# Optimization experiments

Measured on AMD Instinct MI355X. Metric: run time of the kernel, lower is better.

Reference implementation:

```python
import jax, jax.numpy as jnp
import numpy as np

EPS = 1e-8

def setup_inputs() -> dict:
    key = jax.random.key(0)
    ks = jax.random.split(key, 8)
    B, D, N, F = 8192, 1024, 2048, 8
    d2 = D // 2
    # integer-valued data (IDF acts on integers)
    x = jnp.round(jax.random.normal(ks[0], (B, D), jnp.float32) * 5.0)
    s1 = 1.0 / np.sqrt(d2)
    s2 = 1.0 / np.sqrt(N)
    return {
        "x": x,
        "W1": jax.random.normal(ks[1], (F, d2, N), jnp.float32) * s1,
        "b1": jax.random.normal(ks[2], (F, N), jnp.float32) * 0.01,
        "W2": jax.random.normal(ks[3], (F, N, N), jnp.float32) * s2,
        "b2": jax.random.normal(ks[4], (F, N), jnp.float32) * 0.01,
        "W3": jax.random.normal(ks[5], (F, N, d2), jnp.float32) * s2,
        "b3": jax.random.normal(ks[6], (F, d2), jnp.float32) * 0.01,
        "mean": jnp.zeros((1, D), jnp.float32),
        "log_scale": jnp.ones((1, D), jnp.float32),
    }

def _st_round(v):
    # straight-through round: forward round, identity gradient
    return v + jax.lax.stop_gradient(jnp.round(v) - v)

def _flow(x, W1, b1, W2, b2, W3, b3):
    d2 = x.shape[1] // 2
    def step(z, p):
        w1, bb1, w2, bb2, w3, bb3 = p
        xa, xb = z[:, :d2], z[:, d2:]
        h = jax.nn.leaky_relu(xa @ w1 + bb1)          # [B, N]
        h = jax.nn.leaky_relu(h @ w2 + bb2)           # [B, N]
        t = h @ w3 + bb3                               # [B, d2]
        yb = xb + _st_round(t)
        z = jnp.concatenate([xa, yb], axis=1)[:, ::-1]  # coupling + flip permute
        return z, None
    z, _ = jax.lax.scan(step, x, (W1, b1, W2, b2, W3, b3))
    return z

def reference(x, W1, b1, W2, b2, W3, b3, mean, log_scale):
    z = _flow(x, W1, b1, W2, b2, W3, b3)
    # discretized logistic log-prior: log(sig((z+.5-m)/s) - sig((z-.5-m)/s))
    scale = jnp.exp(log_scale)
    la = jax.nn.log_sigmoid((z + 0.5 - mean) / scale)
    lb = jax.nn.log_sigmoid((z - 0.5 - mean) / scale)
    log_p = la + jnp.log(1.0 - jnp.exp(lb - la) + EPS)  # log_min_exp
    return -log_p.sum(axis=1).mean()  # reduction='avg'
```

## Files before the change

### kernel.cpp

```cpp
#include <hip/hip_runtime.h>
#include <hip/hip_bf16.h>
#include <cmath>


typedef __bf16 bf16_t;
typedef bf16_t bf16x8 __attribute__((ext_vector_type(8)));
typedef float floatx4 __attribute__((ext_vector_type(4)));

#define BQ 8192
#define DD 1024
#define D2 512
#define NH 2048
#define NF 8

__device__ __forceinline__ void gload_lds16(const void* g, void* l) {
    __builtin_amdgcn_global_load_lds(
        (__attribute__((address_space(1))) void*)g,
        (__attribute__((address_space(3))) void*)l, 16, 0, 0);
}

__global__ __launch_bounds__(256)
void transpose_bf16(const float* __restrict__ W, bf16_t* __restrict__ Wt,
                    int K, int N) {
    __shared__ float tile[32][33];
    size_t fo = (size_t)blockIdx.z * K * N;
    int n0 = blockIdx.x * 32, k0 = blockIdx.y * 32;
    int tx = threadIdx.x & 31, ty = threadIdx.x >> 5;
    for (int i = 0; i < 4; i++)
        tile[ty + i*8][tx] = W[fo + (size_t)(k0 + ty + i*8) * N + n0 + tx];
    __syncthreads();
    for (int i = 0; i < 4; i++)
        Wt[fo + (size_t)(n0 + ty + i*8) * K + k0 + tx] = (bf16_t)tile[tx][ty + i*8];
}

__global__ __launch_bounds__(256)
void copy_x(const float4* __restrict__ x, float4* __restrict__ S) {
    int idx = blockIdx.x * blockDim.x + threadIdx.x;
    S[idx] = x[idx];
}

__global__ __launch_bounds__(256)
void prep_A(const float* __restrict__ S, bf16_t* __restrict__ Ab, int rflag) {
    int idx = blockIdx.x * blockDim.x + threadIdx.x;
    int m = idx >> 9;
    int j = idx & 511;
    int src = rflag ? (1023 - j) : j;
    Ab[idx] = (bf16_t)S[(size_t)m * DD + src];
}

template<int MODE, int K>
__global__ __launch_bounds__(256)
void gemm_kernel(const bf16_t* __restrict__ A, const bf16_t* __restrict__ Bt,
                 const float* __restrict__ bias,
                 bf16_t* __restrict__ Cout, float* __restrict__ S,
                 int N, int rflag)
{
    __shared__ __align__(16) bf16_t As[2][128 * 32];
    __shared__ __align__(16) bf16_t Bs[2][128 * 32];

    const int tid  = threadIdx.x;
    const int lane = tid & 63;
    const int wave = tid >> 6;
    const int wm   = wave >> 1;
    const int wn   = wave & 1;
    const int m0   = blockIdx.y * 128;
    const int n0   = blockIdx.x * 128;

    const int srow = tid >> 2;
    const int scol = ((tid & 3) ^ ((srow >> 1) & 3)) * 8;
    const bf16_t* ag0 = A  + (size_t)(m0 + srow)      * K + scol;
    const bf16_t* ag1 = A  + (size_t)(m0 + 64 + srow) * K + scol;
    const bf16_t* bg0 = Bt + (size_t)(n0 + srow)      * K + scol;
    const bf16_t* bg1 = Bt + (size_t)(n0 + 64 + srow) * K + scol;

    floatx4 acc[4][4];
#pragma unroll
    for (int i = 0; i < 4; i++)
#pragma unroll
        for (int j = 0; j < 4; j++)
            acc[i][j] = (floatx4){0.f, 0.f, 0.f, 0.f};

    const int fr = lane & 15;
    const int fk = ((lane >> 4) ^ ((fr >> 1) & 3)) * 8;

    gload_lds16(ag0, &As[0][tid * 8]);
    gload_lds16(ag1, &As[0][2048 + tid * 8]);
    gload_lds16(bg0, &Bs[0][tid * 8]);
    gload_lds16(bg1, &Bs[0][2048 + tid * 8]);
    ag0 += 32; ag1 += 32; bg0 += 32; bg1 += 32;

    constexpr int T = K / 32;
#pragma unroll 2
    for (int it = 1; it < T; ++it) {
        __syncthreads();
        const int nb = it & 1;
        const int cb = nb ^ 1;
        gload_lds16(ag0, &As[nb][tid * 8]);
        gload_lds16(ag1, &As[nb][2048 + tid * 8]);
        gload_lds16(bg0, &Bs[nb][tid * 8]);
        gload_lds16(bg1, &Bs[nb][2048 + tid * 8]);
        ag0 += 32; ag1 += 32; bg0 += 32; bg1 += 32;

        bf16x8 af[4], bff[4];
#pragma unroll
        for (int i = 0; i < 4; i++)
            af[i] = *(const bf16x8*)&As[cb][(wm*64 + i*16 + fr) * 32 + fk];
#pragma unroll
        for (int j = 0; j < 4; j++)
            bff[j] = *(const bf16x8*)&Bs[cb][(wn*64 + j*16 + fr) * 32 + fk];
#pragma unroll
        for (int i = 0; i < 4; i++)
#pragma unroll
            for (int j = 0; j < 4; j++)
                acc[i][j] = __builtin_amdgcn_mfma_f32_16x16x32_bf16(
                                af[i], bff[j], acc[i][j], 0, 0, 0);
    }
    __syncthreads();
    {
        const int cb = (T - 1) & 1;
        bf16x8 af[4], bff[4];
#pragma unroll
        for (int i = 0; i < 4; i++)
            af[i] = *(const bf16x8*)&As[cb][(wm*64 + i*16 + fr) * 32 + fk];
#pragma unroll
        for (int j = 0; j < 4; j++)
            bff[j] = *(const bf16x8*)&Bs[cb][(wn*64 + j*16 + fr) * 32 + fk];
#pragma unroll
        for (int i = 0; i < 4; i++)
#pragma unroll
            for (int j = 0; j < 4; j++)
                acc[i][j] = __builtin_amdgcn_mfma_f32_16x16x32_bf16(
                                af[i], bff[j], acc[i][j], 0, 0, 0);
    }

    const int ccol  = lane & 15;
    const int crow4 = (lane >> 4) * 4;
#pragma unroll
    for (int j = 0; j < 4; j++) {
        int col = n0 + wn*64 + j*16 + ccol;
        float bj = bias[col];
        if (MODE == 0) {
#pragma unroll
            for (int i = 0; i < 4; i++) {
#pragma unroll
                for (int r = 0; r < 4; r++) {
                    int row = m0 + wm*64 + i*16 + crow4 + r;
                    float v = acc[i][j][r] + bj;
                    v = v >= 0.f ? v : 0.01f * v;
                    Cout[(size_t)row * N + col] = (bf16_t)v;
                }
            }
        } else {
            int slot = rflag ? (511 - col) : (512 + col);
#pragma unroll
            for (int i = 0; i < 4; i++) {
#pragma unroll
                for (int r = 0; r < 4; r++) {
                    int row = m0 + wm*64 + i*16 + crow4 + r;
                    float t = acc[i][j][r] + bj;
                    float* p = &S[(size_t)row * DD + slot];
                    *p = *p + rintf(t);
                }
            }
        }
    }
}

__global__ __launch_bounds__(256)
void reduce_nll(const float* __restrict__ S, const float* __restrict__ mean,
                const float* __restrict__ log_scale, float* __restrict__ out)
{
    float local = 0.f;
    const int total = BQ * DD;
    for (int idx = blockIdx.x * blockDim.x + threadIdx.x; idx < total;
         idx += gridDim.x * blockDim.x) {
        int j = idx & (DD - 1);
        float z  = S[idx];
        float mu = mean[j];
        float sc = expf(log_scale[j]);
        float ua = (z + 0.5f - mu) / sc;
        float ub = (z - 0.5f - mu) / sc;
        float la = fminf(ua, 0.f) - log1pf(expf(-fabsf(ua)));
        float lb = fminf(ub, 0.f) - log1pf(expf(-fabsf(ub)));
        float lp = la + logf(1.0f - expf(lb - la) + 1e-8f);
        local += lp;
    }
    __shared__ float red[256];
    red[threadIdx.x] = local;
    __syncthreads();
    for (int s = 128; s > 0; s >>= 1) {
        if (threadIdx.x < s) red[threadIdx.x] += red[threadIdx.x + s];
        __syncthreads();
    }
    if (threadIdx.x == 0) atomicAdd(out, -red[0] * (1.0f / (float)BQ));
}

extern "C" void kernel_launch(void* const* d_in, const int* in_sizes, int n_in,
                              void* d_out, int out_size, void* d_ws, size_t ws_size,
                              hipStream_t stream)
{
    const float* x   = (const float*)d_in[0];
    const float* W1  = (const float*)d_in[1];
    const float* b1  = (const float*)d_in[2];
    const float* W2  = (const float*)d_in[3];
    const float* b2  = (const float*)d_in[4];
    const float* W3  = (const float*)d_in[5];
    const float* b3  = (const float*)d_in[6];
    const float* mean = (const float*)d_in[7];
    const float* lsc  = (const float*)d_in[8];

    char* ws = (char*)d_ws;
    bf16_t* Wt1 = (bf16_t*)ws; ws += (size_t)NF * NH * D2 * 2;
    bf16_t* Wt2 = (bf16_t*)ws; ws += (size_t)NF * NH * NH * 2;
    bf16_t* Wt3 = (bf16_t*)ws; ws += (size_t)NF * D2 * NH * 2;
    float*  S   = (float*)ws;  ws += (size_t)BQ * DD * 4;
    bf16_t* Ab  = (bf16_t*)ws; ws += (size_t)BQ * D2 * 2;
    bf16_t* H1  = (bf16_t*)ws; ws += (size_t)BQ * NH * 2;
    bf16_t* H2  = (bf16_t*)ws;

    hipMemsetAsync(d_out, 0, sizeof(float), stream);

    dim3 blk(256);
    transpose_bf16<<<dim3(NH/32, D2/32, NF), blk, 0, stream>>>(W1, Wt1, D2, NH);
    transpose_bf16<<<dim3(NH/32, NH/32, NF), blk, 0, stream>>>(W2, Wt2, NH, NH);
    transpose_bf16<<<dim3(D2/32, NH/32, NF), blk, 0, stream>>>(W3, Wt3, NH, D2);

    copy_x<<<BQ * DD / 4 / 256, blk, 0, stream>>>((const float4*)x, (float4*)S);

    for (int f = 0; f < NF; ++f) {
        int r = f & 1;
        prep_A<<<BQ * D2 / 256, blk, 0, stream>>>(S, Ab, r);
        gemm_kernel<0, D2><<<dim3(NH/128, BQ/128), blk, 0, stream>>>(
            Ab, Wt1 + (size_t)f * NH * D2, b1 + (size_t)f * NH, H1, nullptr,
            NH, 0);
        gemm_kernel<0, NH><<<dim3(NH/128, BQ/128), blk, 0, stream>>>(
            H1, Wt2 + (size_t)f * NH * NH, b2 + (size_t)f * NH, H2, nullptr,
            NH, 0);
        gemm_kernel<1, NH><<<dim3(D2/128, BQ/128), blk, 0, stream>>>(
            H2, Wt3 + (size_t)f * D2 * NH, b3 + (size_t)f * D2, nullptr, S,
            D2, r);
    }

    reduce_nll<<<2048, blk, 0, stream>>>(S, mean, lsc, (float*)d_out);
}
```

Baseline: 1.719 ms.

## Double GEMM K-tile to 64 and fuse next-step operand prep into epilogue

The GEMM now stages 64-wide K slices per iteration with an XOR swizzle over eight 16-byte chunks, halving barrier count per K, and adds an occupancy hint of two blocks per CU. The per-step prep_A kernel is removed. Instead, the third GEMM's epilogue writes the updated, permuted half directly as the bf16 A operand for the next flow step. This costs doubled LDS per block and a few extra scattered bf16 stores in the epilogue.

```diff
diff --git a/kernel.cpp b/kernel.cpp
--- a/kernel.cpp
+++ b/kernel.cpp
@@ -40,23 +40,23 @@
 }
 
 __global__ __launch_bounds__(256)
-void prep_A(const float* __restrict__ S, bf16_t* __restrict__ Ab, int rflag) {
+void prep_A(const float* __restrict__ S, bf16_t* __restrict__ Ab) {
     int idx = blockIdx.x * blockDim.x + threadIdx.x;
     int m = idx >> 9;
     int j = idx & 511;
-    int src = rflag ? (1023 - j) : j;
-    Ab[idx] = (bf16_t)S[(size_t)m * DD + src];
+    Ab[idx] = (bf16_t)S[(size_t)m * DD + j];
 }
 
 template<int MODE, int K>
-__global__ __launch_bounds__(256)
+__global__ __launch_bounds__(256, 2)
 void gemm_kernel(const bf16_t* __restrict__ A, const bf16_t* __restrict__ Bt,
                  const float* __restrict__ bias,
                  bf16_t* __restrict__ Cout, float* __restrict__ S,
+                 bf16_t* __restrict__ Abn,
                  int N, int rflag)
 {
-    __shared__ __align__(16) bf16_t As[2][128 * 32];
-    __shared__ __align__(16) bf16_t Bs[2][128 * 32];
+    __shared__ __align__(16) bf16_t As[2][128 * 64];
+    __shared__ __align__(16) bf16_t Bs[2][128 * 64];
 
     const int tid  = threadIdx.x;
     const int lane = tid & 63;
@@ -66,12 +66,10 @@
     const int m0   = blockIdx.y * 128;
     const int n0   = blockIdx.x * 128;
 
-    const int srow = tid >> 2;
-    const int scol = ((tid & 3) ^ ((srow >> 1) & 3)) * 8;
-    const bf16_t* ag0 = A  + (size_t)(m0 + srow)      * K + scol;
-    const bf16_t* ag1 = A  + (size_t)(m0 + 64 + srow) * K + scol;
-    const bf16_t* bg0 = Bt + (size_t)(n0 + srow)      * K + scol;
-    const bf16_t* bg1 = Bt + (size_t)(n0 + 64 + srow) * K + scol;
+    const int srow = tid >> 3;
+    const int sq   = ((tid & 7) ^ (srow & 7)) * 8;
+    const bf16_t* agp = A  + (size_t)(m0 + srow) * K + sq;
+    const bf16_t* bgp = Bt + (size_t)(n0 + srow) * K + sq;
 
     floatx4 acc[4][4];
 #pragma unroll
@@ -81,56 +79,67 @@
             acc[i][j] = (floatx4){0.f, 0.f, 0.f, 0.f};
 
     const int fr = lane & 15;
-    const int fk = ((lane >> 4) ^ ((fr >> 1) & 3)) * 8;
-
-    gload_lds16(ag0, &As[0][tid * 8]);
-    gload_lds16(ag1, &As[0][2048 + tid * 8]);
-    gload_lds16(bg0, &Bs[0][tid * 8]);
-    gload_lds16(bg1, &Bs[0][2048 + tid * 8]);
-    ag0 += 32; ag1 += 32; bg0 += 32; bg1 += 32;
-
-    constexpr int T = K / 32;
+    const int fq = lane >> 4;
+    const int fx = lane & 7;
+
+#pragma unroll
+    for (int u = 0; u < 4; u++) {
+        gload_lds16(agp + (size_t)(u*32) * K, &As[0][u*2048 + tid*8]);
+        gload_lds16(bgp + (size_t)(u*32) * K, &Bs[0][u*2048 + tid*8]);
+    }
+    agp += 64; bgp += 64;
+
+    constexpr int T = K / 64;
 #pragma unroll 2
     for (int it = 1; it < T; ++it) {
         __syncthreads();
         const int nb = it & 1;
         const int cb = nb ^ 1;
-        gload_lds16(ag0, &As[nb][tid * 8]);
-        gload_lds16(ag1, &As[nb][2048 + tid * 8]);
-        gload_lds16(bg0, &Bs[nb][tid * 8]);
-        gload_lds16(bg1, &Bs[nb][2048 + tid * 8]);
-        ag0 += 32; ag1 += 32; bg0 += 32; bg1 += 32;
-
-        bf16x8 af[4], bff[4];
-#pragma unroll
-        for (int i = 0; i < 4; i++)
-            af[i] = *(const bf16x8*)&As[cb][(wm*64 + i*16 + fr) * 32 + fk];
-#pragma unroll
-        for (int j = 0; j < 4; j++)
-            bff[j] = *(const bf16x8*)&Bs[cb][(wn*64 + j*16 + fr) * 32 + fk];
-#pragma unroll
-        for (int i = 0; i < 4; i++)
+#pragma unroll
+        for (int u = 0; u < 4; u++) {
+            gload_lds16(agp + (size_t)(u*32) * K, &As[nb][u*2048 + tid*8]);
+            gload_lds16(bgp + (size_t)(u*32) * K, &Bs[nb][u*2048 + tid*8]);
+        }
+        agp += 64; bgp += 64;
+
+#pragma unroll
+        for (int s = 0; s < 2; s++) {
+            const int kc = ((s*4 + fq) ^ fx) * 8;
+            bf16x8 af[4], bff[4];
+#pragma unroll
+            for (int i = 0; i < 4; i++)
+                af[i] = *(const bf16x8*)&As[cb][(wm*64 + i*16 + fr) * 64 + kc];
 #pragma unroll
             for (int j = 0; j < 4; j++)
-                acc[i][j] = __builtin_amdgcn_mfma_f32_16x16x32_bf16(
-                                af[i], bff[j], acc[i][j], 0, 0, 0);
+                bff[j] = *(const bf16x8*)&Bs[cb][(wn*64 + j*16 + fr) * 64 + kc];
+#pragma unroll
+            for (int i = 0; i < 4; i++)
+#pragma unroll
+                for (int j = 0; j < 4; j++)
+                    acc[i][j] = __builtin_amdgcn_mfma_f32_16x16x32_bf16(
+                                    af[i], bff[j], acc[i][j], 0, 0, 0);
+        }
     }
     __syncthreads();
     {
         const int cb = (T - 1) & 1;
-        bf16x8 af[4], bff[4];
-#pragma unroll
-        for (int i = 0; i < 4; i++)
-            af[i] = *(const bf16x8*)&As[cb][(wm*64 + i*16 + fr) * 32 + fk];
-#pragma unroll
-        for (int j = 0; j < 4; j++)
-            bff[j] = *(const bf16x8*)&Bs[cb][(wn*64 + j*16 + fr) * 32 + fk];
-#pragma unroll
-        for (int i = 0; i < 4; i++)
+#pragma unroll
+        for (int s = 0; s < 2; s++) {
+            const int kc = ((s*4 + fq) ^ fx) * 8;
+            bf16x8 af[4], bff[4];
+#pragma unroll
+            for (int i = 0; i < 4; i++)
+                af[i] = *(const bf16x8*)&As[cb][(wm*64 + i*16 + fr) * 64 + kc];
 #pragma unroll
             for (int j = 0; j < 4; j++)
-                acc[i][j] = __builtin_amdgcn_mfma_f32_16x16x32_bf16(
-                                af[i], bff[j], acc[i][j], 0, 0, 0);
+                bff[j] = *(const bf16x8*)&Bs[cb][(wn*64 + j*16 + fr) * 64 + kc];
+#pragma unroll
+            for (int i = 0; i < 4; i++)
+#pragma unroll
+                for (int j = 0; j < 4; j++)
+                    acc[i][j] = __builtin_amdgcn_mfma_f32_16x16x32_bf16(
+                                    af[i], bff[j], acc[i][j], 0, 0, 0);
+        }
     }
 
     const int ccol  = lane & 15;
@@ -152,14 +161,16 @@
             }
         } else {
             int slot = rflag ? (511 - col) : (512 + col);
+            int aj   = 511 - col;
 #pragma unroll
             for (int i = 0; i < 4; i++) {
 #pragma unroll
                 for (int r = 0; r < 4; r++) {
                     int row = m0 + wm*64 + i*16 + crow4 + r;
                     float t = acc[i][j][r] + bj;
-                    float* p = &S[(size_t)row * DD + slot];
-                    *p = *p + rintf(t);
+                    float nv = S[(size_t)row * DD + slot] + rintf(t);
+                    S[(size_t)row * DD + slot] = nv;
+                    Abn[(size_t)row * D2 + aj] = (bf16_t)nv;
                 }
             }
         }
@@ -226,19 +237,19 @@
     transpose_bf16<<<dim3(D2/32, NH/32, NF), blk, 0, stream>>>(W3, Wt3, NH, D2);
 
     copy_x<<<BQ * DD / 4 / 256, blk, 0, stream>>>((const float4*)x, (float4*)S);
+    prep_A<<<BQ * D2 / 256, blk, 0, stream>>>(S, Ab);
 
     for (int f = 0; f < NF; ++f) {
         int r = f & 1;
-        prep_A<<<BQ * D2 / 256, blk, 0, stream>>>(S, Ab, r);
         gemm_kernel<0, D2><<<dim3(NH/128, BQ/128), blk, 0, stream>>>(
             Ab, Wt1 + (size_t)f * NH * D2, b1 + (size_t)f * NH, H1, nullptr,
-            NH, 0);
+            nullptr, NH, 0);
         gemm_kernel<0, NH><<<dim3(NH/128, BQ/128), blk, 0, stream>>>(
             H1, Wt2 + (size_t)f * NH * NH, b2 + (size_t)f * NH, H2, nullptr,
-            NH, 0);
+            nullptr, NH, 0);
         gemm_kernel<1, NH><<<dim3(D2/128, BQ/128), blk, 0, stream>>>(
             H2, Wt3 + (size_t)f * D2 * NH, b3 + (size_t)f * D2, nullptr, S,
-            D2, r);
+            Ab, D2, r);
     }
 
     reduce_nll<<<2048, blk, 0, stream>>>(S, mean, lsc, (float*)d_out);
```

Result: faster. 1.619 ms (-5.8%).
